# Optimization experiments

Hardware: AMD Instinct MI355X
Metric: run time of the kernel (lower is better)

The kernel has to match this reference:

```python
import jax, jax.numpy as jnp
import numpy as np

D_MODEL = 2048
NUM_HEADS = 16
HEAD_DIM = D_MODEL // NUM_HEADS


def setup_inputs() -> dict:
    key = jax.random.key(0)
    ks = jax.random.split(key, 11)
    B, S = 2, 2048
    s = 1.0 / np.sqrt(D_MODEL)
    return {
        "query": jax.random.normal(ks[0], (B, S, D_MODEL), jnp.float32),
        "key_in": jax.random.normal(ks[1], (B, S, D_MODEL), jnp.float32),
        "value": jax.random.normal(ks[2], (B, S, D_MODEL), jnp.float32),
        "Wq": jax.random.normal(ks[3], (D_MODEL, D_MODEL), jnp.float32) * s,
        "bq": jnp.zeros((D_MODEL,), jnp.float32),
        "Wk": jax.random.normal(ks[4], (D_MODEL, D_MODEL), jnp.float32) * s,
        "bk": jnp.zeros((D_MODEL,), jnp.float32),
        "Wv": jax.random.normal(ks[5], (D_MODEL, D_MODEL), jnp.float32) * s,
        "bv": jnp.zeros((D_MODEL,), jnp.float32),
        "Wo": jax.random.normal(ks[6], (D_MODEL, D_MODEL), jnp.float32) * s,
        "bo": jnp.zeros((D_MODEL,), jnp.float32),
    }


def reference(query, key_in, value, Wq, bq, Wk, bk, Wv, bv, Wo, bo):
    B, S, _ = query.shape
    # projections (torch Linear: x @ W.T + b)
    q = query @ Wq.T + bq
    k = key_in @ Wk.T + bk
    v = value @ Wv.T + bv
    # [B, H, S, Dh]
    q = q.reshape(B, S, NUM_HEADS, HEAD_DIM).transpose(0, 2, 1, 3)
    k = k.reshape(B, -1, NUM_HEADS, HEAD_DIM).transpose(0, 2, 1, 3)
    v = v.reshape(B, -1, NUM_HEADS, HEAD_DIM).transpose(0, 2, 1, 3)
    scores = jnp.einsum("bhqd,bhkd->bhqk", q, k) / np.sqrt(HEAD_DIM).astype(np.float32)
    attn = jax.nn.softmax(scores, axis=-1)
    out = jnp.einsum("bhqk,bhkd->bhqd", attn, v)
    out = out.transpose(0, 2, 1, 3).reshape(B, S, D_MODEL)
    return out @ Wo.T + bo
```

## Files before the change

kernel.cpp:

```cpp
#include <hip/hip_runtime.h>
#include <hip/hip_bf16.h>
#include <stdint.h>

typedef __hip_bfloat16 bf16;
typedef __attribute__((ext_vector_type(8))) short bf16x8;
typedef __attribute__((ext_vector_type(4))) float f32x4;
typedef __attribute__((ext_vector_type(4))) short s16x4;

constexpr int D_MODEL   = 2048;
constexpr int NUM_HEADS = 16;
constexpr int HEAD_DIM  = 128;
constexpr int BATCH     = 2;
constexpr int SEQ       = 2048;

constexpr int GBM = 256, GBN = 128, GBK = 64;
constexpr int G_ABUF = GBM * GBK;
constexpr int G_BBUF = GBN * GBK;
constexpr int G_BUF  = G_ABUF + G_BBUF;
constexpr int G_LDS  = 3 * G_BUF;

__device__ __forceinline__ void gload_lds16(const bf16* g, bf16* l) {
    __builtin_amdgcn_global_load_lds(
        (const __attribute__((address_space(1))) void*)g,
        (__attribute__((address_space(3))) void*)l, 16, 0, 0);
}

struct CvtArgs { const float* src[7]; bf16* dst[7]; int n8[7]; };

__global__ __launch_bounds__(256)
void cvt_multi(CvtArgs a)
{
    const int t = blockIdx.y;
    const float* __restrict__ s = a.src[t];
    bf16* __restrict__ d = a.dst[t];
    const int n8 = a.n8[t];
    for (int i = blockIdx.x * 256 + threadIdx.x; i < n8; i += gridDim.x * 256) {
        f32x4 x = *(const f32x4*)(s + (size_t)i * 8);
        f32x4 y = *(const f32x4*)(s + (size_t)i * 8 + 4);
        bf16 t8[8] = { __float2bfloat16(x[0]), __float2bfloat16(x[1]),
                       __float2bfloat16(x[2]), __float2bfloat16(x[3]),
                       __float2bfloat16(y[0]), __float2bfloat16(y[1]),
                       __float2bfloat16(y[2]), __float2bfloat16(y[3]) };
        *(bf16x8*)(d + (size_t)i * 8) = *(const bf16x8*)t8;
    }
}

template <typename TC, bool TRANS_PERM>
__device__ __forceinline__
void gemm_body(const bf16* __restrict__ A, const bf16* __restrict__ W,
               const float* __restrict__ bias, TC* __restrict__ C,
               int M, int N, int K, bf16* smem)
{
    const int tid  = threadIdx.x;
    const int lane = tid & 63;
    const int wave = tid >> 6;
    const int quad = lane >> 4, l16 = lane & 15;
    const int sw   = l16 & 7;
    const int wr   = wave >> 1;
    const int wc   = wave & 1;
    const int m0   = blockIdx.y * GBM, n0 = blockIdx.x * GBN;

    const int rloc = tid >> 3;
    const int gsw  = (tid & 7) ^ (rloc & 7);
    const int NT   = K / GBK;

    const bf16* Abase = A + (size_t)(m0 + rloc) * K + gsw * 8;
    const bf16* Bbase = W + (size_t)(n0 + rloc) * K + gsw * 8;
    const size_t rstep = (size_t)64 * K;

    auto stageA = [&](int t, int bi, int u) {
        gload_lds16(Abase + u * rstep + (size_t)t * GBK,
                    smem + bi * G_BUF + (u * 512 + tid) * 8);
    };
    auto stageB = [&](int t, int bi, int u) {
        gload_lds16(Bbase + u * rstep + (size_t)t * GBK,
                    smem + bi * G_BUF + G_ABUF + (u * 512 + tid) * 8);
    };

    f32x4 acc[4][4];
#pragma unroll
    for (int i = 0; i < 4; i++)
#pragma unroll
        for (int j = 0; j < 4; j++) acc[i][j] = (f32x4){0.f, 0.f, 0.f, 0.f};

#pragma unroll
    for (int u = 0; u < 4; u++) stageA(0, 0, u);
#pragma unroll
    for (int u = 0; u < 2; u++) stageB(0, 0, u);
    if (NT > 1) {
#pragma unroll
        for (int u = 0; u < 4; u++) stageA(1, 1, u);
#pragma unroll
        for (int u = 0; u < 2; u++) stageB(1, 1, u);
        asm volatile("s_waitcnt vmcnt(6)" ::: "memory");
    } else {
        asm volatile("s_waitcnt vmcnt(0)" ::: "memory");
    }
    asm volatile("s_barrier" ::: "memory");

    int bc = 0;
    for (int t = 0; t < NT; ++t) {
        const bf16* sAc = smem + bc * G_BUF;
        const bf16* sBc = sAc + G_ABUF;
        const int bs = (bc + 2 >= 3) ? bc - 1 : bc + 2;
        const bool pf = (t + 2 < NT);

        if (pf) {
            stageA(t + 2, bs, 0); stageA(t + 2, bs, 1);
            stageA(t + 2, bs, 2); stageA(t + 2, bs, 3);
            stageB(t + 2, bs, 0); stageB(t + 2, bs, 1);
        }
        __builtin_amdgcn_sched_barrier(0);

        bf16x8 a0[4], b0[4], a1[4], b1[4];
#pragma unroll
        for (int i = 0; i < 4; i++)
            a0[i] = *(const bf16x8*)&sAc[(wr * 64 + i * 16 + l16) * 64 + (quad ^ sw) * 8];
#pragma unroll
        for (int j = 0; j < 4; j++)
            b0[j] = *(const bf16x8*)&sBc[(wc * 64 + j * 16 + l16) * 64 + (quad ^ sw) * 8];
#pragma unroll
        for (int i = 0; i < 4; i++)
            a1[i] = *(const bf16x8*)&sAc[(wr * 64 + i * 16 + l16) * 64 + ((4 + quad) ^ sw) * 8];
#pragma unroll
        for (int j = 0; j < 4; j++)
            b1[j] = *(const bf16x8*)&sBc[(wc * 64 + j * 16 + l16) * 64 + ((4 + quad) ^ sw) * 8];
        __builtin_amdgcn_sched_barrier(0);

        __builtin_amdgcn_s_setprio(1);
#pragma unroll
        for (int i = 0; i < 4; i++)
#pragma unroll
            for (int j = 0; j < 4; j++)
                acc[i][j] = __builtin_amdgcn_mfma_f32_16x16x32_bf16(a0[i], b0[j], acc[i][j], 0, 0, 0);
#pragma unroll
        for (int i = 0; i < 4; i++)
#pragma unroll
            for (int j = 0; j < 4; j++)
                acc[i][j] = __builtin_amdgcn_mfma_f32_16x16x32_bf16(a1[i], b1[j], acc[i][j], 0, 0, 0);
        __builtin_amdgcn_s_setprio(0);

        if (pf)                asm volatile("s_waitcnt vmcnt(6)" ::: "memory");
        else if (t + 1 < NT)   asm volatile("s_waitcnt vmcnt(0)" ::: "memory");
        asm volatile("s_barrier" ::: "memory");
        bc = (bc + 1 == 3) ? 0 : bc + 1;
    }

#pragma unroll
    for (int j = 0; j < 4; j++) {
        const int col = n0 + wc * 64 + j * 16 + l16;
        const float bv = bias[col];
#pragma unroll
        for (int i = 0; i < 4; i++) {
            const int row0 = m0 + wr * 64 + i * 16 + quad * 4;
            if constexpr (TRANS_PERM) {
                int g   = row0 & 63;
                int tau = g >> 4, qh = (g >> 2) & 3;
                int pp  = (tau >> 1) * 32 + qh * 8 + (tau & 1) * 4;
                int sp  = ((row0 & 2047) & ~63) | pp;
                size_t idx = (size_t)(row0 >> 11) * ((size_t)D_MODEL * SEQ)
                           + (size_t)col * SEQ + sp;
                bf16 t4[4];
#pragma unroll
                for (int r = 0; r < 4; r++) t4[r] = __float2bfloat16(acc[i][j][r] + bv);
                *(s16x4*)&C[idx] = *(const s16x4*)t4;
            } else {
#pragma unroll
                for (int r = 0; r < 4; r++) {
                    int row = row0 + r;
                    if constexpr (sizeof(TC) == 2)
                        C[(size_t)row * N + col] = (TC)__float2bfloat16(acc[i][j][r] + bv);
                    else
                        C[(size_t)row * N + col] = (TC)(acc[i][j][r] + bv);
                }
            }
        }
    }
}

template <typename TC, bool TRANS_PERM>
__global__ __launch_bounds__(512, 1)
void gemm_bf16(const bf16* __restrict__ A, const bf16* __restrict__ W,
               const float* __restrict__ bias, TC* __restrict__ C,
               int M, int N, int K)
{
    __shared__ bf16 smem[G_LDS];
    gemm_body<TC, TRANS_PERM>(A, W, bias, C, M, N, K, smem);
}

struct QkvArgs { const bf16* A[3]; const bf16* W[3]; const float* bias[3]; bf16* C[3]; };

__global__ __launch_bounds__(512, 1)
void gemm_qkv(QkvArgs ga, int M, int N, int K)
{
    __shared__ bf16 smem[G_LDS];
    const int z = blockIdx.z;
    if (z == 2) gemm_body<bf16, true >(ga.A[2], ga.W[2], ga.bias[2], ga.C[2], M, N, K, smem);
    else        gemm_body<bf16, false>(ga.A[z], ga.W[z], ga.bias[z], ga.C[z], M, N, K, smem);
}

struct QkArgs { const bf16* A[2]; const bf16* W[2]; const float* bias[2]; bf16* C[2]; };

__global__ __launch_bounds__(512, 1)
void gemm_qk(QkArgs ga, int M, int N, int K)
{
    __shared__ bf16 smem[G_LDS];
    const int z = blockIdx.z;
    gemm_body<bf16, false>(ga.A[z], ga.W[z], ga.bias[z], ga.C[z], M, N, K, smem);
}

__global__ __launch_bounds__(256)
void flash_attn_kernel(const bf16* __restrict__ Qp, const bf16* __restrict__ Kp,
                       const bf16* __restrict__ Vt, bf16* __restrict__ Op)
{
    constexpr int BQ = 128, BKV = 64, DH = 128;
    __shared__ bf16 sK[2][BKV * DH];
    __shared__ bf16 sV[2][DH * BKV];

    const int tid  = threadIdx.x;
    const int wave = tid >> 6, lane = tid & 63;
    const int quad = lane >> 4, l16 = lane & 15;
    const int q0 = blockIdx.x * BQ;
    const int h  = blockIdx.y;
    const int b  = blockIdx.z;

    const size_t base  = (size_t)b * SEQ * D_MODEL + (size_t)h * HEAD_DIM;
    const size_t basev = ((size_t)b * NUM_HEADS + h) * (size_t)HEAD_DIM * SEQ;
    const bf16* Kb = Kp + base;
    const bf16* Vb = Vt + basev;

    auto stage = [&](int t, int bi) {
        const bf16* Kt = Kb + (size_t)t * BKV * D_MODEL;
        const bf16* Vtile = Vb + (size_t)t * BKV;
        bf16* sKb = sK[bi];
        bf16* sVb = sV[bi];
#pragma unroll
        for (int s = 0; s < 4; s++) {
            int c = s * 256 + wave * 64 + lane;
            int row = c >> 4, gs = c & 15;
            int g = gs ^ (row & 15);
            gload_lds16(Kt + (size_t)row * D_MODEL + g * 8, sKb + (size_t)c * 8);
        }
#pragma unroll
        for (int s = 0; s < 4; s++) {
            int c = s * 256 + wave * 64 + lane;
            int dh = c >> 3, gs = c & 7;
            int g = gs ^ (dh & 7);
            gload_lds16(Vtile + (size_t)dh * SEQ + g * 8, sVb + (size_t)c * 8);
        }
    };

    bf16x8 bq[2][4];
#pragma unroll
    for (int nt = 0; nt < 2; nt++)
#pragma unroll
        for (int kk = 0; kk < 4; kk++)
            bq[nt][kk] = *(const bf16x8*)&Qp[base +
                (size_t)(q0 + wave * 32 + nt * 16 + l16) * D_MODEL + kk * 32 + quad * 8];

    f32x4 oacc[2][8];
#pragma unroll
    for (int nt = 0; nt < 2; nt++)
#pragma unroll
        for (int mt = 0; mt < 8; mt++) oacc[nt][mt] = (f32x4){0.f, 0.f, 0.f, 0.f};

    float lsum[2] = {0.f, 0.f};

    const float SCL2E = 0.08838834764831845f * 1.4426950408889634f;
    constexpr int NT = SEQ / BKV;

    stage(0, 0);

    for (int t = 0; t < NT; ++t) {
        __syncthreads();
        if (t + 1 < NT) stage(t + 1, (t + 1) & 1);

        const bf16* sKc = sK[t & 1];
        const bf16* sVc = sV[t & 1];

        f32x4 sacc[2][4];
#pragma unroll
        for (int nt = 0; nt < 2; nt++)
#pragma unroll
            for (int kt = 0; kt < 4; kt++) sacc[nt][kt] = (f32x4){0.f, 0.f, 0.f, 0.f};
#pragma unroll
        for (int kk = 0; kk < 4; kk++) {
            bf16x8 ak[4];
#pragma unroll
            for (int kt = 0; kt < 4; kt++) {
                int row = kt * 16 + l16;
                int g   = (kk * 4 + quad) ^ l16;
                ak[kt] = *(const bf16x8*)&sKc[(size_t)row * DH + g * 8];
            }
#pragma unroll
            for (int nt = 0; nt < 2; nt++)
#pragma unroll
                for (int kt = 0; kt < 4; kt++)
                    sacc[nt][kt] = __builtin_amdgcn_mfma_f32_16x16x32_bf16(ak[kt], bq[nt][kk], sacc[nt][kt], 0, 0, 0);
        }

        bf16x8 pb[2][2];
#pragma unroll
        for (int nt = 0; nt < 2; nt++) {
            bf16 tmp[16];
#pragma unroll
            for (int kt = 0; kt < 4; kt++) {
#pragma unroll
                for (int r = 0; r < 4; r++) {
                    float p = exp2f(fminf(sacc[nt][kt][r] * SCL2E, 60.f));
                    lsum[nt] += p;
                    tmp[(kt >> 1) * 8 + (kt & 1) * 4 + r] = __float2bfloat16(p);
                }
            }
            pb[nt][0] = *(const bf16x8*)&tmp[0];
            pb[nt][1] = *(const bf16x8*)&tmp[8];
        }

#pragma unroll
        for (int c = 0; c < 2; c++) {
#pragma unroll
            for (int mt = 0; mt < 8; mt++) {
                int row = mt * 16 + l16;
                int g   = (c * 4 + quad) ^ (l16 & 7);
                bf16x8 av = *(const bf16x8*)&sVc[(size_t)row * BKV + g * 8];
#pragma unroll
                for (int nt = 0; nt < 2; nt++)
                    oacc[nt][mt] = __builtin_amdgcn_mfma_f32_16x16x32_bf16(av, pb[nt][c], oacc[nt][mt], 0, 0, 0);
            }
        }
    }

#pragma unroll
    for (int nt = 0; nt < 2; nt++) {
        float v = lsum[nt];
        v += __shfl_xor(v, 16);
        v += __shfl_xor(v, 32);
        lsum[nt] = v;
    }

#pragma unroll
    for (int nt = 0; nt < 2; nt++) {
        float inv = 1.f / lsum[nt];
        int row = q0 + wave * 32 + nt * 16 + l16;
#pragma unroll
        for (int mt = 0; mt < 8; mt++) {
            bf16 t4[4];
#pragma unroll
            for (int r = 0; r < 4; r++) t4[r] = __float2bfloat16(oacc[nt][mt][r] * inv);
            *(s16x4*)&Op[base + (size_t)row * D_MODEL + mt * 16 + quad * 4] = *(const s16x4*)t4;
        }
    }
}

extern "C" void kernel_launch(void* const* d_in, const int* in_sizes, int n_in,
                              void* d_out, int out_size, void* d_ws, size_t ws_size,
                              hipStream_t stream)
{
    const float* query  = (const float*)d_in[0];
    const float* key_in = (const float*)d_in[1];
    const float* value  = (const float*)d_in[2];
    const float* Wq = (const float*)d_in[3];
    const float* bq = (const float*)d_in[4];
    const float* Wk = (const float*)d_in[5];
    const float* bk = (const float*)d_in[6];
    const float* Wv = (const float*)d_in[7];
    const float* bv = (const float*)d_in[8];
    const float* Wo = (const float*)d_in[9];
    const float* bo = (const float*)d_in[10];
    float* out = (float*)d_out;

    const int tokens = BATCH * SEQ;
    const size_t nAct = (size_t)tokens * D_MODEL;
    const size_t nW   = (size_t)D_MODEL * D_MODEL;

    const bool fused_qkv = ws_size >= (6 * nAct + 4 * nW) * sizeof(bf16);

    bf16* p = (bf16*)d_ws;
    bf16* qb  = p; p += nAct;
    bf16* kb  = p; p += nAct;
    bf16* vb  = p; p += nAct;
    bf16* wqb = p; p += nW;
    bf16* wkb = p; p += nW;
    bf16* wvb = p; p += nW;
    bf16* wob = p; p += nW;
    bf16* qp  = p; p += nAct;
    bf16* kp  = p; p += nAct;
    bf16* vpT;
    if (fused_qkv) { vpT = p; p += nAct; }
    else           { vpT = qb; }
    bf16* ap = fused_qkv ? qb : kb;

    CvtArgs ca;
    ca.src[0] = query;  ca.dst[0] = qb;  ca.n8[0] = (int)(nAct / 8);
    ca.src[1] = key_in; ca.dst[1] = kb;  ca.n8[1] = (int)(nAct / 8);
    ca.src[2] = value;  ca.dst[2] = vb;  ca.n8[2] = (int)(nAct / 8);
    ca.src[3] = Wq;     ca.dst[3] = wqb; ca.n8[3] = (int)(nW / 8);
    ca.src[4] = Wk;     ca.dst[4] = wkb; ca.n8[4] = (int)(nW / 8);
    ca.src[5] = Wv;     ca.dst[5] = wvb; ca.n8[5] = (int)(nW / 8);
    ca.src[6] = Wo;     ca.dst[6] = wob; ca.n8[6] = (int)(nW / 8);
    cvt_multi<<<dim3(512, 7), 256, 0, stream>>>(ca);

    if (fused_qkv) {
        QkvArgs qa;
        qa.A[0] = qb; qa.W[0] = wqb; qa.bias[0] = bq; qa.C[0] = qp;
        qa.A[1] = kb; qa.W[1] = wkb; qa.bias[1] = bk; qa.C[1] = kp;
        qa.A[2] = vb; qa.W[2] = wvb; qa.bias[2] = bv; qa.C[2] = vpT;
        dim3 g3(D_MODEL / 128, tokens / 256, 3);
        gemm_qkv<<<g3, 512, 0, stream>>>(qa, tokens, D_MODEL, D_MODEL);
    } else {
        QkArgs qa;
        qa.A[0] = qb; qa.W[0] = wqb; qa.bias[0] = bq; qa.C[0] = qp;
        qa.A[1] = kb; qa.W[1] = wkb; qa.bias[1] = bk; qa.C[1] = kp;
        dim3 g2(D_MODEL / 128, tokens / 256, 2);
        gemm_qk<<<g2, 512, 0, stream>>>(qa, tokens, D_MODEL, D_MODEL);
        dim3 gg(D_MODEL / 128, tokens / 256);
        gemm_bf16<bf16, true><<<gg, 512, 0, stream>>>(vb, wvb, bv, vpT, tokens, D_MODEL, D_MODEL);
    }

    dim3 ga(SEQ / 128, NUM_HEADS, BATCH);
    flash_attn_kernel<<<ga, 256, 0, stream>>>(qp, kp, vpT, ap);

    dim3 gg(D_MODEL / 128, tokens / 256);
    gemm_bf16<float, false><<<gg, 512, 0, stream>>>(ap, wob, bo, out, tokens, D_MODEL, D_MODEL);
}
```

Before: 449.1 us.

## Hand-issue GEMM LDS reads in inline asm and split waitcnt across MFMA halves

The GEMM inner loop now computes per-thread LDS byte offsets once and issues all 16 ds_read_b128 loads in one inline asm block using immediate offsets. It waits on lgkmcnt(8) before the first half of the MFMAs and lgkmcnt(0) before the second half, so the second half of the fragment reads overlaps with compute. Launch bounds on the GEMM kernels change from 1 to 2 blocks per CU, which limits registers per thread. LDS use of about 144 KB per block may still prevent a second block from fitting, and the tighter register budget risks spills.

After: 455.3 us. No clear change (+1.4%).

```diff
diff --git a/kernel.cpp b/kernel.cpp
--- a/kernel.cpp
+++ b/kernel.cpp
@@ -24,6 +24,8 @@
         (const __attribute__((address_space(1))) void*)g,
         (__attribute__((address_space(3))) void*)l, 16, 0, 0);
 }
+
+typedef __attribute__((address_space(3))) const bf16 lds_cbf16;
 
 struct CvtArgs { const float* src[7]; bf16* dst[7]; int n8[7]; };
 
@@ -77,6 +79,11 @@
                     smem + bi * G_BUF + G_ABUF + (u * 512 + tid) * 8);
     };
 
+    const uint32_t aoffTh = (uint32_t)(uintptr_t)(lds_cbf16*)
+        &smem[(wr * 64 + l16) * 64 + (quad ^ sw) * 8];
+    const uint32_t boffTh = (uint32_t)(uintptr_t)(lds_cbf16*)
+        &smem[G_ABUF + (wc * 64 + l16) * 64 + (quad ^ sw) * 8];
+
     f32x4 acc[4][4];
 #pragma unroll
     for (int i = 0; i < 4; i++)
@@ -100,8 +107,6 @@
 
     int bc = 0;
     for (int t = 0; t < NT; ++t) {
-        const bf16* sAc = smem + bc * G_BUF;
-        const bf16* sBc = sAc + G_ABUF;
         const int bs = (bc + 2 >= 3) ? bc - 1 : bc + 2;
         const bool pf = (t + 2 < NT);
 
@@ -112,27 +117,47 @@
         }
         __builtin_amdgcn_sched_barrier(0);
 
+        const uint32_t vA0 = aoffTh + (uint32_t)(bc * (G_BUF * 2));
+        const uint32_t vB0 = boffTh + (uint32_t)(bc * (G_BUF * 2));
+        const uint32_t vA1 = vA0 ^ 64u;
+        const uint32_t vB1 = vB0 ^ 64u;
         bf16x8 a0[4], b0[4], a1[4], b1[4];
-#pragma unroll
-        for (int i = 0; i < 4; i++)
-            a0[i] = *(const bf16x8*)&sAc[(wr * 64 + i * 16 + l16) * 64 + (quad ^ sw) * 8];
-#pragma unroll
-        for (int j = 0; j < 4; j++)
-            b0[j] = *(const bf16x8*)&sBc[(wc * 64 + j * 16 + l16) * 64 + (quad ^ sw) * 8];
-#pragma unroll
-        for (int i = 0; i < 4; i++)
-            a1[i] = *(const bf16x8*)&sAc[(wr * 64 + i * 16 + l16) * 64 + ((4 + quad) ^ sw) * 8];
-#pragma unroll
-        for (int j = 0; j < 4; j++)
-            b1[j] = *(const bf16x8*)&sBc[(wc * 64 + j * 16 + l16) * 64 + ((4 + quad) ^ sw) * 8];
+        asm volatile(
+            "ds_read_b128 %0, %16 offset:0\n\t"
+            "ds_read_b128 %1, %16 offset:2048\n\t"
+            "ds_read_b128 %2, %16 offset:4096\n\t"
+            "ds_read_b128 %3, %16 offset:6144\n\t"
+            "ds_read_b128 %4, %17 offset:0\n\t"
+            "ds_read_b128 %5, %17 offset:2048\n\t"
+            "ds_read_b128 %6, %17 offset:4096\n\t"
+            "ds_read_b128 %7, %17 offset:6144\n\t"
+            "ds_read_b128 %8, %18 offset:0\n\t"
+            "ds_read_b128 %9, %18 offset:2048\n\t"
+            "ds_read_b128 %10, %18 offset:4096\n\t"
+            "ds_read_b128 %11, %18 offset:6144\n\t"
+            "ds_read_b128 %12, %19 offset:0\n\t"
+            "ds_read_b128 %13, %19 offset:2048\n\t"
+            "ds_read_b128 %14, %19 offset:4096\n\t"
+            "ds_read_b128 %15, %19 offset:6144"
+            : "=&v"(a0[0]), "=&v"(a0[1]), "=&v"(a0[2]), "=&v"(a0[3]),
+              "=&v"(b0[0]), "=&v"(b0[1]), "=&v"(b0[2]), "=&v"(b0[3]),
+              "=&v"(a1[0]), "=&v"(a1[1]), "=&v"(a1[2]), "=&v"(a1[3]),
+              "=&v"(b1[0]), "=&v"(b1[1]), "=&v"(b1[2]), "=&v"(b1[3])
+            : "v"(vA0), "v"(vB0), "v"(vA1), "v"(vB1));
+
+        asm volatile("s_waitcnt lgkmcnt(8)" ::: "memory");
         __builtin_amdgcn_sched_barrier(0);
-
         __builtin_amdgcn_s_setprio(1);
 #pragma unroll
         for (int i = 0; i < 4; i++)
 #pragma unroll
             for (int j = 0; j < 4; j++)
                 acc[i][j] = __builtin_amdgcn_mfma_f32_16x16x32_bf16(a0[i], b0[j], acc[i][j], 0, 0, 0);
+        __builtin_amdgcn_s_setprio(0);
+
+        asm volatile("s_waitcnt lgkmcnt(0)" ::: "memory");
+        __builtin_amdgcn_sched_barrier(0);
+        __builtin_amdgcn_s_setprio(1);
 #pragma unroll
         for (int i = 0; i < 4; i++)
 #pragma unroll
@@ -179,7 +204,7 @@
 }
 
 template <typename TC, bool TRANS_PERM>
-__global__ __launch_bounds__(512, 1)
+__global__ __launch_bounds__(512, 2)
 void gemm_bf16(const bf16* __restrict__ A, const bf16* __restrict__ W,
                const float* __restrict__ bias, TC* __restrict__ C,
                int M, int N, int K)
@@ -190,7 +215,7 @@
 
 struct QkvArgs { const bf16* A[3]; const bf16* W[3]; const float* bias[3]; bf16* C[3]; };
 
-__global__ __launch_bounds__(512, 1)
+__global__ __launch_bounds__(512, 2)
 void gemm_qkv(QkvArgs ga, int M, int N, int K)
 {
     __shared__ bf16 smem[G_LDS];
@@ -201,7 +226,7 @@
 
 struct QkArgs { const bf16* A[2]; const bf16* W[2]; const float* bias[2]; bf16* C[2]; };
 
-__global__ __launch_bounds__(512, 1)
+__global__ __launch_bounds__(512, 2)
 void gemm_qk(QkArgs ga, int M, int N, int K)
 {
     __shared__ bf16 smem[G_LDS];
```
